# Performance work log

Hardware: AMD Instinct MI355X
Metric: run time of the kernel (lower is better)

## Reference

```python
import jax, jax.numpy as jnp
import numpy as np

B, N, C, H, W, D = 2, 6, 3, 64, 176, 64


def setup_inputs() -> dict:
    key = jax.random.key(0)
    k1, k2, k3 = jax.random.split(key, 3)
    image_features = jax.random.normal(k1, (B * N, C, H, W), dtype=jnp.float32)
    # Realistic pinhole intrinsics (invertible 3x3 upper-left block), with small
    # multiplicative jitter that preserves the sparsity pattern / invertibility.
    K = jnp.array([[500.0, 0.0, W / 2.0, 0.0],
                   [0.0, 500.0, H / 2.0, 0.0],
                   [0.0, 0.0, 1.0, 0.0],
                   [0.0, 0.0, 0.0, 1.0]], dtype=jnp.float32)
    jitter = 1.0 + 0.01 * jax.random.normal(k2, (B, N, 4, 4), dtype=jnp.float32)
    intrinsics = K * jitter  # (B, N, 4, 4)
    extrinsics = jax.random.normal(k3, (B, N, 4, 4), dtype=jnp.float32)
    # Buffers created in the torch __init__ (meshgrid with indexing='ij'):
    ys, xs = jnp.meshgrid(jnp.arange(H, dtype=jnp.float32),
                          jnp.arange(W, dtype=jnp.float32), indexing='ij')
    xy1 = jnp.stack([xs.ravel(), ys.ravel(), jnp.ones(H * W, dtype=jnp.float32)], axis=0)  # (3, HW)
    depths = jnp.linspace(0.1, 1.0, D, dtype=jnp.float32)  # (D,)
    return {"image_features": image_features, "intrinsics": intrinsics,
            "extrinsics": extrinsics, "xy1": xy1, "depths": depths}


def reference(image_features, intrinsics, extrinsics, xy1, depths):
    BN, C_, H_, W_ = image_features.shape
    B_, N_ = intrinsics.shape[:2]
    D_ = depths.shape[0]
    feat = image_features.reshape(B_, N_, C_, H_ * W_)  # (B,N,C,HW)
    # Camera rays: K^{-1} @ [x, y, 1]
    K_inv = jnp.linalg.inv(intrinsics[:, :, :3, :3])  # (B,N,3,3)
    rays = jnp.einsum('bnij,jp->bnip', K_inv, xy1)  # (B,N,3,HW)
    # Depth probabilities: softmax over the flattened spatial dim (as in source)
    probs = jax.nn.softmax(feat, axis=3)  # (B,N,C,HW)
    depth_map = probs[..., None] * depths  # (B,N,C,HW,D)
    # Outer product of rays with per-depth weights (C must be 3 for broadcast)
    point_cloud = rays[..., None] * depth_map  # (B,N,3,HW,D)
    ones = jnp.ones_like(point_cloud[:, :, :1])
    hom = jnp.concatenate([point_cloud, ones], axis=2)  # (B,N,4,HW,D)
    # Tiny 4x4 extrinsics transform over a huge pointwise batch
    world = jnp.einsum('bnij,bnjpd->bnipd', extrinsics, hom)[:, :, :3]  # (B,N,3,HW,D)
    return world.reshape(B_, N_, 3, H_, W_, D_)
```

## Files before the change

### kernel.cpp

```cpp
#include <hip/hip_runtime.h>
#include <hip/hip_bf16.h>


#define BN   12
#define CCH  3
#define HH   64
#define WW   176
#define HWSZ (HH * WW)
#define DD   64
#define PIX  16
#define TILES (HWSZ / PIX)

__global__ __launch_bounds__(256) void lss_softmax_stats(
    const float* __restrict__ feat, float* __restrict__ mx_out,
    float* __restrict__ invsum_out) {
  const int row = blockIdx.x;
  const int t = threadIdx.x;
  const float4* rp = (const float4*)(feat + (size_t)row * HWSZ);

  float4 v[11];
  float m = -3.4e38f;
#pragma unroll
  for (int k = 0; k < 11; ++k) {
    v[k] = rp[t + 256 * k];
    m = fmaxf(m, fmaxf(fmaxf(v[k].x, v[k].y), fmaxf(v[k].z, v[k].w)));
  }
#pragma unroll
  for (int off = 32; off > 0; off >>= 1) m = fmaxf(m, __shfl_down(m, off, 64));

  __shared__ float smax[4];
  __shared__ float ssum[4];
  const int wave = t >> 6, lane = t & 63;
  if (lane == 0) smax[wave] = m;
  __syncthreads();
  if (t == 0)
    smax[0] = fmaxf(fmaxf(smax[0], smax[1]), fmaxf(smax[2], smax[3]));
  __syncthreads();
  m = smax[0];

  float s = 0.f;
#pragma unroll
  for (int k = 0; k < 11; ++k) {
    s += __expf(v[k].x - m) + __expf(v[k].y - m) + __expf(v[k].z - m) +
         __expf(v[k].w - m);
  }
#pragma unroll
  for (int off = 32; off > 0; off >>= 1) s += __shfl_down(s, off, 64);
  if (lane == 0) ssum[wave] = s;
  __syncthreads();
  if (t == 0) {
    mx_out[row] = m;
    invsum_out[row] = 1.0f / (ssum[0] + ssum[1] + ssum[2] + ssum[3]);
  }
}

__global__ __launch_bounds__(256) void lss_main(
    const float* __restrict__ feat, const float* __restrict__ intr,
    const float* __restrict__ extr, const float* __restrict__ depths,
    const float* __restrict__ mx, const float* __restrict__ invsum,
    float* __restrict__ out) {
  const int blk = blockIdx.x;
  const int bn = blk / TILES;
  const int tile = blk - bn * TILES;
  const int p0 = tile * PIX;
  const int t = threadIdx.x;

  __shared__ float s_s[PIX][4];
  __shared__ float s_a[PIX][4];

  const float* Kp = intr + bn * 16;
  const float a = Kp[0], b = Kp[1], c = Kp[2];
  const float d = Kp[4], e = Kp[5], f = Kp[6];
  const float g = Kp[8], h = Kp[9], i9 = Kp[10];
  const float A0 = e * i9 - f * h;
  const float B0 = -(d * i9 - f * g);
  const float C0 = d * h - e * g;
  const float invdet = 1.0f / (a * A0 + b * B0 + c * C0);
  const float inv00 = A0 * invdet, inv01 = -(b * i9 - c * h) * invdet,
              inv02 = (b * f - c * e) * invdet;
  const float inv10 = B0 * invdet, inv11 = (a * i9 - c * g) * invdet,
              inv12 = -(a * f - c * d) * invdet;
  const float inv20 = C0 * invdet, inv21 = -(a * h - b * g) * invdet,
              inv22 = (a * e - b * d) * invdet;

  const float* Ep = extr + bn * 16;

  if (t < 48) {
    const int cc = t >> 4;
    const int pl = t & 15;
    const int p = p0 + pl;
    const float fv = feat[((size_t)bn * CCH + cc) * HWSZ + p];
    const float prob = __expf(fv - mx[bn * CCH + cc]) * invsum[bn * CCH + cc];
    const float x = (float)(p % WW);
    const float y = (float)(p / WW);
    float ray;
    if (cc == 0)      ray = inv00 * x + inv01 * y + inv02;
    else if (cc == 1) ray = inv10 * x + inv11 * y + inv12;
    else              ray = inv20 * x + inv21 * y + inv22;
    s_s[pl][cc] = ray * prob;
  }
  __syncthreads();
  if (t < 48) {
    const int ii = t >> 4;
    const int pl = t & 15;
    s_a[pl][ii] = Ep[ii * 4 + 0] * s_s[pl][0] + Ep[ii * 4 + 1] * s_s[pl][1] +
                  Ep[ii * 4 + 2] * s_s[pl][2];
  }
  __syncthreads();

  const int pl = t >> 4;
  const int dq = t & 15;
  const int p = p0 + pl;
  const float4 dep = ((const float4*)depths)[dq];
#pragma unroll
  for (int ii = 0; ii < 3; ++ii) {
    const float av = s_a[pl][ii];
    const float tr = Ep[ii * 4 + 3];
    float4 o;
    o.x = av * dep.x + tr;
    o.y = av * dep.y + tr;
    o.z = av * dep.z + tr;
    o.w = av * dep.w + tr;
    ((float4*)out)[(((size_t)bn * CCH + ii) * HWSZ + p) * (DD / 4) + dq] = o;
  }
}

extern "C" void kernel_launch(void* const* d_in, const int* in_sizes, int n_in,
                              void* d_out, int out_size, void* d_ws,
                              size_t ws_size, hipStream_t stream) {
  const float* feat = (const float*)d_in[0];
  const float* intr = (const float*)d_in[1];
  const float* extr = (const float*)d_in[2];
  const float* depths = (const float*)d_in[4];
  float* out = (float*)d_out;

  float* mx = (float*)d_ws;
  float* invsum = mx + 64;

  lss_softmax_stats<<<BN * CCH, 256, 0, stream>>>(feat, mx, invsum);
  lss_main<<<BN * TILES, 256, 0, stream>>>(feat, intr, extr, depths, mx,
                                           invsum, out);
}
```

Measured before the change: 121.1 us.

## Enlarge pixel tiles, use nontemporal stores, widen softmax-stats blocks

The main kernel now handles 64 pixels per block instead of 16, so there are a quarter as many blocks. It drops one barrier and shared-memory stage by folding the extrinsic 3x3 transform into each thread's store loop, and writes the large output with nontemporal stores. The softmax-stats kernel uses 704 threads per row so each thread holds fewer registers. The aim is to cut block scheduling overhead, idle threads and cache pollution on this write-bound kernel. The cost is that each thread recomputes the small transform per pixel and the total number of blocks drops.

```diff
diff --git a/kernel.cpp b/kernel.cpp
--- a/kernel.cpp
+++ b/kernel.cpp
@@ -2,45 +2,52 @@
 #include <hip/hip_bf16.h>
 
 
-#define BN   12
-#define CCH  3
-#define HH   64
-#define WW   176
-#define HWSZ (HH * WW)
-#define DD   64
-#define PIX  16
+#define BN    12
+#define CCH   3
+#define HH    64
+#define WW    176
+#define HWSZ  (HH * WW)
+#define DD    64
+#define PIX   64
 #define TILES (HWSZ / PIX)
 
-__global__ __launch_bounds__(256) void lss_softmax_stats(
+typedef float fvec4 __attribute__((ext_vector_type(4)));
+
+__global__ __launch_bounds__(704) void lss_softmax_stats(
     const float* __restrict__ feat, float* __restrict__ mx_out,
     float* __restrict__ invsum_out) {
   const int row = blockIdx.x;
   const int t = threadIdx.x;
-  const float4* rp = (const float4*)(feat + (size_t)row * HWSZ);
+  const fvec4* rp = (const fvec4*)(feat + (size_t)row * HWSZ);
 
-  float4 v[11];
+  fvec4 v[4];
   float m = -3.4e38f;
 #pragma unroll
-  for (int k = 0; k < 11; ++k) {
-    v[k] = rp[t + 256 * k];
+  for (int k = 0; k < 4; ++k) {
+    v[k] = rp[t + 704 * k];
     m = fmaxf(m, fmaxf(fmaxf(v[k].x, v[k].y), fmaxf(v[k].z, v[k].w)));
   }
 #pragma unroll
   for (int off = 32; off > 0; off >>= 1) m = fmaxf(m, __shfl_down(m, off, 64));
 
-  __shared__ float smax[4];
-  __shared__ float ssum[4];
+  __shared__ float smax[11];
+  __shared__ float ssum[11];
+  __shared__ float sbcast;
   const int wave = t >> 6, lane = t & 63;
   if (lane == 0) smax[wave] = m;
   __syncthreads();
-  if (t == 0)
-    smax[0] = fmaxf(fmaxf(smax[0], smax[1]), fmaxf(smax[2], smax[3]));
+  if (t == 0) {
+    float mm = smax[0];
+#pragma unroll
+    for (int w = 1; w < 11; ++w) mm = fmaxf(mm, smax[w]);
+    sbcast = mm;
+  }
   __syncthreads();
-  m = smax[0];
+  m = sbcast;
 
   float s = 0.f;
 #pragma unroll
-  for (int k = 0; k < 11; ++k) {
+  for (int k = 0; k < 4; ++k) {
     s += __expf(v[k].x - m) + __expf(v[k].y - m) + __expf(v[k].z - m) +
          __expf(v[k].w - m);
   }
@@ -49,8 +56,11 @@
   if (lane == 0) ssum[wave] = s;
   __syncthreads();
   if (t == 0) {
+    float ss = 0.f;
+#pragma unroll
+    for (int w = 0; w < 11; ++w) ss += ssum[w];
     mx_out[row] = m;
-    invsum_out[row] = 1.0f / (ssum[0] + ssum[1] + ssum[2] + ssum[3]);
+    invsum_out[row] = 1.0f / ss;
   }
 }
 
@@ -65,8 +75,7 @@
   const int p0 = tile * PIX;
   const int t = threadIdx.x;
 
-  __shared__ float s_s[PIX][4];
-  __shared__ float s_a[PIX][4];
+  __shared__ float s_s[CCH][PIX];
 
   const float* Kp = intr + bn * 16;
   const float a = Kp[0], b = Kp[1], c = Kp[2];
@@ -76,52 +85,61 @@
   const float B0 = -(d * i9 - f * g);
   const float C0 = d * h - e * g;
   const float invdet = 1.0f / (a * A0 + b * B0 + c * C0);
-  const float inv00 = A0 * invdet, inv01 = -(b * i9 - c * h) * invdet,
-              inv02 = (b * f - c * e) * invdet;
-  const float inv10 = B0 * invdet, inv11 = (a * i9 - c * g) * invdet,
-              inv12 = -(a * f - c * d) * invdet;
-  const float inv20 = C0 * invdet, inv21 = -(a * h - b * g) * invdet,
-              inv22 = (a * e - b * d) * invdet;
 
-  const float* Ep = extr + bn * 16;
-
-  if (t < 48) {
-    const int cc = t >> 4;
-    const int pl = t & 15;
+  if (t < 192) {
+    const int cc = t >> 6;
+    const int pl = t & 63;
     const int p = p0 + pl;
     const float fv = feat[((size_t)bn * CCH + cc) * HWSZ + p];
     const float prob = __expf(fv - mx[bn * CCH + cc]) * invsum[bn * CCH + cc];
     const float x = (float)(p % WW);
     const float y = (float)(p / WW);
-    float ray;
-    if (cc == 0)      ray = inv00 * x + inv01 * y + inv02;
-    else if (cc == 1) ray = inv10 * x + inv11 * y + inv12;
-    else              ray = inv20 * x + inv21 * y + inv22;
-    s_s[pl][cc] = ray * prob;
+    float r0, r1, r2;
+    if (cc == 0) {
+      r0 = A0 * invdet; r1 = -(b * i9 - c * h) * invdet;
+      r2 = (b * f - c * e) * invdet;
+    } else if (cc == 1) {
+      r0 = B0 * invdet; r1 = (a * i9 - c * g) * invdet;
+      r2 = -(a * f - c * d) * invdet;
+    } else {
+      r0 = C0 * invdet; r1 = -(a * h - b * g) * invdet;
+      r2 = (a * e - b * d) * invdet;
+    }
+    s_s[cc][pl] = (r0 * x + r1 * y + r2) * prob;
   }
-  __syncthreads();
-  if (t < 48) {
-    const int ii = t >> 4;
-    const int pl = t & 15;
-    s_a[pl][ii] = Ep[ii * 4 + 0] * s_s[pl][0] + Ep[ii * 4 + 1] * s_s[pl][1] +
-                  Ep[ii * 4 + 2] * s_s[pl][2];
-  }
+
+  const float* Ep = extr + bn * 16;
+  const float e00 = Ep[0], e01 = Ep[1], e02 = Ep[2], e03 = Ep[3];
+  const float e10 = Ep[4], e11 = Ep[5], e12 = Ep[6], e13 = Ep[7];
+  const float e20 = Ep[8], e21 = Ep[9], e22 = Ep[10], e23 = Ep[11];
+
   __syncthreads();
 
-  const int pl = t >> 4;
   const int dq = t & 15;
-  const int p = p0 + pl;
-  const float4 dep = ((const float4*)depths)[dq];
+  const int plb = t >> 4;
+  const fvec4 dep = ((const fvec4*)depths)[dq];
+  fvec4* outq = (fvec4*)out;
+  const size_t base0 = ((size_t)(bn * CCH + 0) * HWSZ + p0) * (DD / 4) + dq;
+  const size_t base1 = ((size_t)(bn * CCH + 1) * HWSZ + p0) * (DD / 4) + dq;
+  const size_t base2 = ((size_t)(bn * CCH + 2) * HWSZ + p0) * (DD / 4) + dq;
+
 #pragma unroll
-  for (int ii = 0; ii < 3; ++ii) {
-    const float av = s_a[pl][ii];
-    const float tr = Ep[ii * 4 + 3];
-    float4 o;
-    o.x = av * dep.x + tr;
-    o.y = av * dep.y + tr;
-    o.z = av * dep.z + tr;
-    o.w = av * dep.w + tr;
-    ((float4*)out)[(((size_t)bn * CCH + ii) * HWSZ + p) * (DD / 4) + dq] = o;
+  for (int gq = 0; gq < 4; ++gq) {
+    const int pl = gq * 16 + plb;
+    const float s0 = s_s[0][pl], s1 = s_s[1][pl], s2 = s_s[2][pl];
+    const float a0 = e00 * s0 + e01 * s1 + e02 * s2;
+    const float a1 = e10 * s0 + e11 * s1 + e12 * s2;
+    const float a2 = e20 * s0 + e21 * s1 + e22 * s2;
+    fvec4 o;
+    o.x = a0 * dep.x + e03; o.y = a0 * dep.y + e03;
+    o.z = a0 * dep.z + e03; o.w = a0 * dep.w + e03;
+    __builtin_nontemporal_store(o, &outq[base0 + (size_t)pl * (DD / 4)]);
+    o.x = a1 * dep.x + e13; o.y = a1 * dep.y + e13;
+    o.z = a1 * dep.z + e13; o.w = a1 * dep.w + e13;
+    __builtin_nontemporal_store(o, &outq[base1 + (size_t)pl * (DD / 4)]);
+    o.x = a2 * dep.x + e23; o.y = a2 * dep.y + e23;
+    o.z = a2 * dep.z + e23; o.w = a2 * dep.w + e23;
+    __builtin_nontemporal_store(o, &outq[base2 + (size_t)pl * (DD / 4)]);
   }
 }
 
@@ -137,7 +155,7 @@
   float* mx = (float*)d_ws;
   float* invsum = mx + 64;
 
-  lss_softmax_stats<<<BN * CCH, 256, 0, stream>>>(feat, mx, invsum);
+  lss_softmax_stats<<<BN * CCH, 704, 0, stream>>>(feat, mx, invsum);
   lss_main<<<BN * TILES, 256, 0, stream>>>(feat, intr, extr, depths, mx,
                                            invsum, out);
 }
```

Result: slower. 123.9 us (+2.3%).
